# Kernel optimization log

Hardware: AMD Instinct MI355X
Metric: run time of the kernel (lower is better)

The kernel has to match this reference:

```python
import jax, jax.numpy as jnp
import numpy as np

B, F, V, E, D_DENSE = 16384, 26, 100000, 16, 13
HIDDEN = [256, 128]
DNN_IN = F * E + D_DENSE  # 429
INIT_STD = 1e-4


def setup_inputs() -> dict:
    key = jax.random.key(0)
    ks = jax.random.split(key, 12)
    X_sparse = jax.random.randint(ks[0], (B, F), 0, V, dtype=jnp.int32)
    X_dense = jax.random.normal(ks[1], (B, D_DENSE), dtype=jnp.float32)
    # Per-field embedding tables stacked: [F, V, dim]
    lin_emb_w = jax.random.normal(ks[2], (F, V, 1), dtype=jnp.float32) * 0.01
    fm_emb_w = jax.random.normal(ks[3], (F, V, E), dtype=jnp.float32) * 0.01
    dense_w = jax.random.normal(ks[4], (1, D_DENSE), dtype=jnp.float32) * 0.01
    dense_b = jnp.zeros((1,), dtype=jnp.float32)
    W1 = jax.random.normal(ks[5], (HIDDEN[0], DNN_IN), dtype=jnp.float32) * INIT_STD
    b1 = jnp.zeros((HIDDEN[0],), dtype=jnp.float32)
    W2 = jax.random.normal(ks[6], (HIDDEN[1], HIDDEN[0]), dtype=jnp.float32) * INIT_STD
    b2 = jnp.zeros((HIDDEN[1],), dtype=jnp.float32)
    Wout = jax.random.normal(ks[7], (1, HIDDEN[1]), dtype=jnp.float32) * 0.01
    return {"X_sparse": X_sparse, "X_dense": X_dense, "lin_emb_w": lin_emb_w,
            "fm_emb_w": fm_emb_w, "dense_w": dense_w, "dense_b": dense_b,
            "W1": W1, "b1": b1, "W2": W2, "b2": b2, "Wout": Wout}


def reference(X_sparse, X_dense, lin_emb_w, fm_emb_w, dense_w, dense_b,
              W1, b1, W2, b2, Wout):
    f_idx = jnp.arange(F)[None, :]  # broadcast field index against [B, F]
    # --- FM linear (1st order) part ---
    lin_sparse = lin_emb_w[f_idx, X_sparse]            # [B, F, 1]
    lin_sparse = jnp.sum(lin_sparse, axis=1)           # [B, 1]
    lin_dense = X_dense @ dense_w.T + dense_b          # [B, 1]
    linear_part = lin_sparse + lin_dense
    # --- FM 2nd-order cross term ---
    fm = fm_emb_w[f_idx, X_sparse]                     # [B, F, E]
    sum_emb = jnp.sum(fm, axis=1)                      # [B, E]
    square_of_sum = sum_emb * sum_emb
    sum_of_square = jnp.sum(fm * fm, axis=1)
    cross = 0.5 * jnp.sum(square_of_sum - sum_of_square, axis=1, keepdims=True)
    fm_logit = linear_part + cross                     # [B, 1]
    # --- DNN part (dropout identity: eval mode) ---
    h = jnp.concatenate([fm.reshape(B, F * E), X_dense], axis=1)  # [B, 429]
    h = jax.nn.relu(h @ W1.T + b1)
    h = jax.nn.relu(h @ W2.T + b2)
    dnn_logit = h @ Wout.T                             # [B, 1]
    out = jax.nn.sigmoid(fm_logit + dnn_logit)
    return out.squeeze(1)                              # [B]
```

## Files before the change

kernel.cpp:

```cpp
#include <hip/hip_runtime.h>
#include <hip/hip_bf16.h>
#include <math.h>

#define BTOT   16384
#define NF     26
#define VOCAB  100000
#define EDIM   16
#define DD     13
#define KPAD   448
#define KREAL  429
#define N1     256
#define N2     128
#define SPB    32
#define APAD   456
#define H2PAD  264

typedef __attribute__((ext_vector_type(8))) short bf16x8;
typedef __attribute__((ext_vector_type(4))) short bf16x4;
typedef __attribute__((ext_vector_type(4))) float f32x4;

static __device__ __forceinline__ bf16x8 ldb8(const __hip_bfloat16* p) {
  return *reinterpret_cast<const bf16x8*>(p);
}
static __device__ __forceinline__ short f2bf(float f) {
  __hip_bfloat16 h = __float2bfloat16(f);
  return *reinterpret_cast<short*>(&h);
}

__global__ __launch_bounds__(512) void convert_weights(
    const float* __restrict__ W1, const float* __restrict__ W2,
    __hip_bfloat16* __restrict__ W1f, __hip_bfloat16* __restrict__ W2f) {
  const int bid = blockIdx.x;
  const int k = threadIdx.x;
  if (bid < 256) {
    const int n = bid;
    if (k < 448) {
      float v = (k < KREAL) ? W1[(size_t)n * KREAL + k] : 0.f;
      W1f[(((size_t)(k >> 3)) * N1 + n) * 8 + (k & 7)] = __float2bfloat16(v);
    }
  } else {
    const int n = bid - 256;
    if (k < 256) {
      float v = W2[(size_t)n * 256 + k];
      W2f[(((size_t)(k >> 3)) * N2 + n) * 8 + (k & 7)] = __float2bfloat16(v);
    }
  }
}

__global__ __launch_bounds__(1024, 8) void deepfm_fused(
    const int* __restrict__ Xs, const float* __restrict__ Xd,
    const float* __restrict__ linW, const float* __restrict__ fmW,
    const float* __restrict__ denseW, const float* __restrict__ denseB,
    const __hip_bfloat16* __restrict__ W1f, const float* __restrict__ b1,
    const __hip_bfloat16* __restrict__ W2f, const float* __restrict__ b2,
    const float* __restrict__ Wout, float* __restrict__ out) {

  __shared__ __hip_bfloat16 Ash[SPB][APAD];
  __shared__ __hip_bfloat16 H2sh[SPB][H2PAD];
  __shared__ float fmlsh[SPB];
  __shared__ float redsh[SPB][8];

  const int tid = threadIdx.x;
  const size_t blk0 = (size_t)blockIdx.x * SPB;

  {
    const int s   = tid >> 5;
    const int sub = tid & 31;
    const int q   = sub & 3;
    const int g   = sub >> 2;
    const size_t b = blk0 + s;
    const int* xrow = Xs + b * NF;

    int idxs[4];
#pragma unroll
    for (int i = 0; i < 4; ++i) {
      int f = g + 8 * i;
      idxs[i] = (f < NF) ? xrow[f] : 0;
    }

    f32x4 sum = (f32x4){0.f, 0.f, 0.f, 0.f};
    f32x4 sumsq = (f32x4){0.f, 0.f, 0.f, 0.f};
    float part = 0.f;

#pragma unroll
    for (int i = 0; i < 4; ++i) {
      const int f = g + 8 * i;
      if (f < NF) {
        const float* row = fmW + ((size_t)f * VOCAB + idxs[i]) * EDIM;
        f32x4 v = *reinterpret_cast<const f32x4*>(row + q * 4);
        sum += v;
        sumsq += v * v;
        bf16x4 pk;
        pk[0] = f2bf(v[0]); pk[1] = f2bf(v[1]);
        pk[2] = f2bf(v[2]); pk[3] = f2bf(v[3]);
        *reinterpret_cast<bf16x4*>(&Ash[s][f * EDIM + q * 4]) = pk;
        if (q == (i & 3))
          part += linW[(size_t)f * VOCAB + idxs[i]];
      }
    }
#pragma unroll
    for (int off = 4; off <= 16; off <<= 1) {
#pragma unroll
      for (int c = 0; c < 4; ++c) {
        sum[c] += __shfl_xor(sum[c], off);
        sumsq[c] += __shfl_xor(sumsq[c], off);
      }
    }
    if (g == 0) {
      f32x4 c4 = sum * sum - sumsq;
      part += 0.5f * (c4[0] + c4[1] + c4[2] + c4[3]);
    }
    float xd = (sub < DD) ? Xd[b * DD + sub] : 0.f;
    Ash[s][416 + sub] = __float2bfloat16(xd);
    if (sub < DD) part += xd * denseW[sub];
#pragma unroll
    for (int off = 1; off < 32; off <<= 1)
      part += __shfl_xor(part, off);
    if (sub == 0) fmlsh[s] = part + denseB[0];
  }
  __syncthreads();

  const int wave = tid >> 6;
  const int lane = tid & 63;
  const int lr = lane & 15;
  const int kg = lane >> 4;
  {
    const int n0 = wave * 16;
    f32x4 acc[2];
    acc[0] = (f32x4){0.f, 0.f, 0.f, 0.f};
    acc[1] = (f32x4){0.f, 0.f, 0.f, 0.f};

#pragma unroll
    for (int kt = 0; kt < KPAD / 32; ++kt) {
      const int kbase = kt * 32 + kg * 8;
      bf16x8 bf = ldb8(W1f + ((size_t)(kbase >> 3) * N1 + n0 + lr) * 8);
#pragma unroll
      for (int mt = 0; mt < 2; ++mt) {
        bf16x8 af = *reinterpret_cast<const bf16x8*>(&Ash[mt * 16 + lr][kbase]);
        acc[mt] = __builtin_amdgcn_mfma_f32_16x16x32_bf16(af, bf, acc[mt], 0, 0, 0);
      }
    }
    const int col = n0 + lr;
    const float bias = b1[col];
#pragma unroll
    for (int mt = 0; mt < 2; ++mt) {
#pragma unroll
      for (int r = 0; r < 4; ++r) {
        float v = acc[mt][r] + bias;
        v = v > 0.f ? v : 0.f;
        H2sh[mt * 16 + kg * 4 + r][col] = __float2bfloat16(v);
      }
    }
  }
  __syncthreads();

  {
    const int c  = wave & 7;
    const int h  = wave >> 3;
    const int n0 = c * 16;
    f32x4 acc = (f32x4){0.f, 0.f, 0.f, 0.f};

#pragma unroll
    for (int kt = 0; kt < N1 / 32; ++kt) {
      const int kbase = kt * 32 + kg * 8;
      bf16x8 bf = ldb8(W2f + ((size_t)(kbase >> 3) * N2 + n0 + lr) * 8);
      bf16x8 af = *reinterpret_cast<const bf16x8*>(&H2sh[h * 16 + lr][kbase]);
      acc = __builtin_amdgcn_mfma_f32_16x16x32_bf16(af, bf, acc, 0, 0, 0);
    }
    const float w0 = Wout[n0 + lr];
    const float bb0 = b2[n0 + lr];
#pragma unroll
    for (int r = 0; r < 4; ++r) {
      float v = acc[r] + bb0;
      v = v > 0.f ? v : 0.f;
      v *= w0;
#pragma unroll
      for (int off = 1; off < 16; off <<= 1)
        v += __shfl_xor(v, off);
      if (lr == 0) redsh[h * 16 + kg * 4 + r][c] = v;
    }
  }
  __syncthreads();

  if (tid < SPB) {
    const int row = tid;
    float t = 0.f;
#pragma unroll
    for (int w = 0; w < 8; ++w) t += redsh[row][w];
    float x = fmlsh[row] + t;
    out[blk0 + row] = 1.f / (1.f + expf(-x));
  }
}

extern "C" void kernel_launch(void* const* d_in, const int* in_sizes, int n_in,
                              void* d_out, int out_size, void* d_ws, size_t ws_size,
                              hipStream_t stream) {
  const int*   Xs   = (const int*)d_in[0];
  const float* Xd   = (const float*)d_in[1];
  const float* linW = (const float*)d_in[2];
  const float* fmW  = (const float*)d_in[3];
  const float* dW   = (const float*)d_in[4];
  const float* dB   = (const float*)d_in[5];
  const float* W1   = (const float*)d_in[6];
  const float* b1   = (const float*)d_in[7];
  const float* W2   = (const float*)d_in[8];
  const float* b2   = (const float*)d_in[9];
  const float* Wout = (const float*)d_in[10];
  float* out = (float*)d_out;

  char* ws = (char*)d_ws;
  __hip_bfloat16* W1f = (__hip_bfloat16*)(ws);
  __hip_bfloat16* W2f = (__hip_bfloat16*)(ws + 229376);

  convert_weights<<<384, 512, 0, stream>>>(W1, W2, W1f, W2f);
  deepfm_fused<<<BTOT / SPB, 1024, 0, stream>>>(
      Xs, Xd, linW, fmW, dW, dB, W1f, b1, W2f, b2, Wout, out);
}
```

Measured before the change: 34.36 us.

## Halve block size and overlap embedding gather with MLP stages across waves

The block shrinks from 1024 to 512 threads and its 32 samples are processed in two halves of 16. While waves 0-3 gather embeddings for the second half, waves 4-7 run the first GEMM on the first half. Next, waves 0-3 run GEMM1 on the second half while waves 4-7 run GEMM2 on the first. All waves then finish GEMM2 for the second half. The aim is to hide the latency of the random embedding gathers behind MFMA work. The cost is more work per wave (four N tiles each), more block phases, and the first gather phase still running alone.

```diff
diff --git a/kernel.cpp b/kernel.cpp
--- a/kernel.cpp
+++ b/kernel.cpp
@@ -47,7 +47,83 @@
   }
 }
 
-__global__ __launch_bounds__(1024, 8) void deepfm_fused(
+
+__device__ __forceinline__ void gemm1_chunk(
+    int r0, int w4, int lane,
+    const __hip_bfloat16 (*Ash)[APAD], __hip_bfloat16 (*H2sh)[H2PAD],
+    const __hip_bfloat16* __restrict__ W1f, const float* __restrict__ b1) {
+  const int lr = lane & 15;
+  const int kg = lane >> 4;
+  const int n0 = w4 * 64;
+  f32x4 acc[4];
+#pragma unroll
+  for (int nt = 0; nt < 4; ++nt) acc[nt] = (f32x4){0.f, 0.f, 0.f, 0.f};
+
+#pragma unroll
+  for (int kt = 0; kt < KPAD / 32; ++kt) {
+    const int kbase = kt * 32 + kg * 8;
+    bf16x8 af = *reinterpret_cast<const bf16x8*>(&Ash[r0 + lr][kbase]);
+#pragma unroll
+    for (int nt = 0; nt < 4; ++nt) {
+      bf16x8 bf = ldb8(W1f + ((size_t)(kbase >> 3) * N1 + n0 + nt * 16 + lr) * 8);
+      acc[nt] = __builtin_amdgcn_mfma_f32_16x16x32_bf16(af, bf, acc[nt], 0, 0, 0);
+    }
+  }
+#pragma unroll
+  for (int nt = 0; nt < 4; ++nt) {
+    const int col = n0 + nt * 16 + lr;
+    const float bias = b1[col];
+#pragma unroll
+    for (int r = 0; r < 4; ++r) {
+      float v = acc[nt][r] + bias;
+      v = v > 0.f ? v : 0.f;
+      H2sh[r0 + kg * 4 + r][col] = __float2bfloat16(v);
+    }
+  }
+}
+
+template <int NWAVES>
+__device__ __forceinline__ void gemm2_chunk(
+    int r0, int wl, int lane,
+    const __hip_bfloat16 (*H2sh)[H2PAD], float (*redsh)[8],
+    const __hip_bfloat16* __restrict__ W2f, const float* __restrict__ b2,
+    const float* __restrict__ Wout) {
+  const int lr = lane & 15;
+  const int kg = lane >> 4;
+  constexpr int NT = 128 / (16 * NWAVES);
+  const int n0 = wl * NT * 16;
+  f32x4 acc[NT];
+#pragma unroll
+  for (int nt = 0; nt < NT; ++nt) acc[nt] = (f32x4){0.f, 0.f, 0.f, 0.f};
+
+#pragma unroll
+  for (int kt = 0; kt < N1 / 32; ++kt) {
+    const int kbase = kt * 32 + kg * 8;
+    bf16x8 af = *reinterpret_cast<const bf16x8*>(&H2sh[r0 + lr][kbase]);
+#pragma unroll
+    for (int nt = 0; nt < NT; ++nt) {
+      bf16x8 bf = ldb8(W2f + ((size_t)(kbase >> 3) * N2 + n0 + nt * 16 + lr) * 8);
+      acc[nt] = __builtin_amdgcn_mfma_f32_16x16x32_bf16(af, bf, acc[nt], 0, 0, 0);
+    }
+  }
+#pragma unroll
+  for (int r = 0; r < 4; ++r) {
+    float v = 0.f;
+#pragma unroll
+    for (int nt = 0; nt < NT; ++nt) {
+      const int col = n0 + nt * 16 + lr;
+      float t = acc[nt][r] + b2[col];
+      t = t > 0.f ? t : 0.f;
+      v += t * Wout[col];
+    }
+#pragma unroll
+    for (int off = 1; off < 16; off <<= 1)
+      v += __shfl_xor(v, off);
+    if (lr == 0) redsh[r0 + kg * 4 + r][wl] = v;
+  }
+}
+
+__global__ __launch_bounds__(512, 4) void deepfm_fused(
     const int* __restrict__ Xs, const float* __restrict__ Xd,
     const float* __restrict__ linW, const float* __restrict__ fmW,
     const float* __restrict__ denseW, const float* __restrict__ denseB,
@@ -61,6 +137,8 @@
   __shared__ float redsh[SPB][8];
 
   const int tid = threadIdx.x;
+  const int wave = tid >> 6;
+  const int lane = tid & 63;
   const size_t blk0 = (size_t)blockIdx.x * SPB;
 
   {
@@ -77,19 +155,71 @@
       int f = g + 8 * i;
       idxs[i] = (f < NF) ? xrow[f] : 0;
     }
-
     f32x4 sum = (f32x4){0.f, 0.f, 0.f, 0.f};
     f32x4 sumsq = (f32x4){0.f, 0.f, 0.f, 0.f};
     float part = 0.f;
-
 #pragma unroll
     for (int i = 0; i < 4; ++i) {
       const int f = g + 8 * i;
       if (f < NF) {
         const float* row = fmW + ((size_t)f * VOCAB + idxs[i]) * EDIM;
         f32x4 v = *reinterpret_cast<const f32x4*>(row + q * 4);
-        sum += v;
-        sumsq += v * v;
+        sum += v; sumsq += v * v;
+        bf16x4 pk;
+        pk[0] = f2bf(v[0]); pk[1] = f2bf(v[1]);
+        pk[2] = f2bf(v[2]); pk[3] = f2bf(v[3]);
+        *reinterpret_cast<bf16x4*>(&Ash[s][f * EDIM + q * 4]) = pk;
+        if (q == i)
+          part += linW[(size_t)f * VOCAB + idxs[i]];
+      }
+    }
+#pragma unroll
+    for (int off = 4; off <= 16; off <<= 1) {
+#pragma unroll
+      for (int c = 0; c < 4; ++c) {
+        sum[c] += __shfl_xor(sum[c], off);
+        sumsq[c] += __shfl_xor(sumsq[c], off);
+      }
+    }
+    if (g == 0) {
+      f32x4 c4 = sum * sum - sumsq;
+      part += 0.5f * (c4[0] + c4[1] + c4[2] + c4[3]);
+    }
+    float xd = (sub < DD) ? Xd[b * DD + sub] : 0.f;
+    Ash[s][416 + sub] = __float2bfloat16(xd);
+    if (sub < DD) part += xd * denseW[sub];
+#pragma unroll
+    for (int off = 1; off < 32; off <<= 1)
+      part += __shfl_xor(part, off);
+    if (sub == 0) fmlsh[s] = part + denseB[0];
+  }
+  __syncthreads();
+
+  if (wave < 4) {
+    const int t   = tid;
+    const int s   = 16 + (t >> 4);
+    const int sub = t & 15;
+    const int q   = sub & 3;
+    const int g   = sub >> 2;
+    const size_t b = blk0 + s;
+    const int* xrow = Xs + b * NF;
+
+    int idxs[7];
+#pragma unroll
+    for (int i = 0; i < 7; ++i) {
+      int f = g + 4 * i;
+      idxs[i] = (f < NF) ? xrow[f] : 0;
+    }
+    f32x4 sum = (f32x4){0.f, 0.f, 0.f, 0.f};
+    f32x4 sumsq = (f32x4){0.f, 0.f, 0.f, 0.f};
+    float part = 0.f;
+#pragma unroll
+    for (int i = 0; i < 7; ++i) {
+      const int f = g + 4 * i;
+      if (f < NF) {
+        const float* row = fmW + ((size_t)f * VOCAB + idxs[i]) * EDIM;
+        f32x4 v = *reinterpret_cast<const f32x4*>(row + q * 4);
+        sum += v; sumsq += v * v;
         bf16x4 pk;
         pk[0] = f2bf(v[0]); pk[1] = f2bf(v[1]);
         pk[2] = f2bf(v[2]); pk[3] = f2bf(v[3]);
@@ -99,7 +229,7 @@
       }
     }
 #pragma unroll
-    for (int off = 4; off <= 16; off <<= 1) {
+    for (int off = 4; off <= 8; off <<= 1) {
 #pragma unroll
       for (int c = 0; c < 4; ++c) {
         sum[c] += __shfl_xor(sum[c], off);
@@ -112,81 +242,32 @@
     }
     float xd = (sub < DD) ? Xd[b * DD + sub] : 0.f;
     Ash[s][416 + sub] = __float2bfloat16(xd);
+    Ash[s][432 + sub] = __float2bfloat16(0.f);
     if (sub < DD) part += xd * denseW[sub];
 #pragma unroll
-    for (int off = 1; off < 32; off <<= 1)
+    for (int off = 1; off < 16; off <<= 1)
       part += __shfl_xor(part, off);
     if (sub == 0) fmlsh[s] = part + denseB[0];
-  }
-  __syncthreads();
-
-  const int wave = tid >> 6;
-  const int lane = tid & 63;
-  const int lr = lane & 15;
-  const int kg = lane >> 4;
-  {
-    const int n0 = wave * 16;
-    f32x4 acc[2];
-    acc[0] = (f32x4){0.f, 0.f, 0.f, 0.f};
-    acc[1] = (f32x4){0.f, 0.f, 0.f, 0.f};
-
-#pragma unroll
-    for (int kt = 0; kt < KPAD / 32; ++kt) {
-      const int kbase = kt * 32 + kg * 8;
-      bf16x8 bf = ldb8(W1f + ((size_t)(kbase >> 3) * N1 + n0 + lr) * 8);
-#pragma unroll
-      for (int mt = 0; mt < 2; ++mt) {
-        bf16x8 af = *reinterpret_cast<const bf16x8*>(&Ash[mt * 16 + lr][kbase]);
-        acc[mt] = __builtin_amdgcn_mfma_f32_16x16x32_bf16(af, bf, acc[mt], 0, 0, 0);
-      }
-    }
-    const int col = n0 + lr;
-    const float bias = b1[col];
-#pragma unroll
-    for (int mt = 0; mt < 2; ++mt) {
-#pragma unroll
-      for (int r = 0; r < 4; ++r) {
-        float v = acc[mt][r] + bias;
-        v = v > 0.f ? v : 0.f;
-        H2sh[mt * 16 + kg * 4 + r][col] = __float2bfloat16(v);
-      }
-    }
-  }
-  __syncthreads();
-
-  {
-    const int c  = wave & 7;
-    const int h  = wave >> 3;
-    const int n0 = c * 16;
-    f32x4 acc = (f32x4){0.f, 0.f, 0.f, 0.f};
-
-#pragma unroll
-    for (int kt = 0; kt < N1 / 32; ++kt) {
-      const int kbase = kt * 32 + kg * 8;
-      bf16x8 bf = ldb8(W2f + ((size_t)(kbase >> 3) * N2 + n0 + lr) * 8);
-      bf16x8 af = *reinterpret_cast<const bf16x8*>(&H2sh[h * 16 + lr][kbase]);
-      acc = __builtin_amdgcn_mfma_f32_16x16x32_bf16(af, bf, acc, 0, 0, 0);
-    }
-    const float w0 = Wout[n0 + lr];
-    const float bb0 = b2[n0 + lr];
-#pragma unroll
-    for (int r = 0; r < 4; ++r) {
-      float v = acc[r] + bb0;
-      v = v > 0.f ? v : 0.f;
-      v *= w0;
-#pragma unroll
-      for (int off = 1; off < 16; off <<= 1)
-        v += __shfl_xor(v, off);
-      if (lr == 0) redsh[h * 16 + kg * 4 + r][c] = v;
-    }
-  }
+  } else {
+    gemm1_chunk(0, wave - 4, lane, Ash, H2sh, W1f, b1);
+  }
+  __syncthreads();
+
+  if (wave < 4) {
+    gemm1_chunk(16, wave, lane, Ash, H2sh, W1f, b1);
+  } else {
+    gemm2_chunk<4>(0, wave - 4, lane, H2sh, redsh, W2f, b2, Wout);
+  }
+  __syncthreads();
+
+  gemm2_chunk<8>(16, wave, lane, H2sh, redsh, W2f, b2, Wout);
   __syncthreads();
 
   if (tid < SPB) {
     const int row = tid;
+    const int nslots = (row < 16) ? 4 : 8;
     float t = 0.f;
-#pragma unroll
-    for (int w = 0; w < 8; ++w) t += redsh[row][w];
+    for (int w = 0; w < nslots; ++w) t += redsh[row][w];
     float x = fmlsh[row] + t;
     out[blk0 + row] = 1.f / (1.f + expf(-x));
   }
@@ -213,6 +294,6 @@
   __hip_bfloat16* W2f = (__hip_bfloat16*)(ws + 229376);
 
   convert_weights<<<384, 512, 0, stream>>>(W1, W2, W1f, W2f);
-  deepfm_fused<<<BTOT / SPB, 1024, 0, stream>>>(
+  deepfm_fused<<<BTOT / SPB, 512, 0, stream>>>(
       Xs, Xd, linW, fmW, dW, dB, W1f, b1, W2f, b2, Wout, out);
 }
```

Measured after the change: 35.85 us. 4.4% more time.

## Process two sample tiles per block and prefetch the second tile's gathers

Applied to the files above, without the earlier changes.

Each block now handles 64 samples as two 32-sample tiles. The embedding gathers for both tiles are issued up front, so the second tile's gather latency can hide behind the first tile's MLP GEMMs. The first tile's barriers wait only on LDS traffic (lgkmcnt), not on the outstanding global loads. This halves the grid and lowers the launch-bounds occupancy hint, and it raises register pressure, which may reduce latency hiding across blocks.

```diff
diff --git a/kernel.cpp b/kernel.cpp
--- a/kernel.cpp
+++ b/kernel.cpp
@@ -11,7 +11,6 @@
 #define KREAL  429
 #define N1     256
 #define N2     128
-#define SPB    32
 #define APAD   456
 #define H2PAD  264
 
@@ -26,6 +25,12 @@
   __hip_bfloat16 h = __float2bfloat16(f);
   return *reinterpret_cast<short*>(&h);
 }
+
+#define LGKM_BAR() do {                                   \
+  asm volatile("s_waitcnt lgkmcnt(0)" ::: "memory");      \
+  __builtin_amdgcn_s_barrier();                           \
+  asm volatile("" ::: "memory");                          \
+} while (0)
 
 __global__ __launch_bounds__(512) void convert_weights(
     const float* __restrict__ W1, const float* __restrict__ W2,
@@ -47,148 +52,199 @@
   }
 }
 
-__global__ __launch_bounds__(1024, 8) void deepfm_fused(
+__device__ __forceinline__ void gather_issue(
+    int g, int q, const int idxs[4],
+    const float* __restrict__ fmW, const float* __restrict__ linW,
+    f32x4 v[4], float& lin) {
+  lin = 0.f;
+#pragma unroll
+  for (int i = 0; i < 4; ++i) {
+    const int f = g + 8 * i;
+    if (f < NF) {
+      v[i] = *reinterpret_cast<const f32x4*>(
+          fmW + ((size_t)f * VOCAB + idxs[i]) * EDIM + q * 4);
+      if (q == i)
+        lin = linW[(size_t)f * VOCAB + idxs[i]];
+    }
+  }
+}
+
+__device__ __forceinline__ void build_tile(
+    int s, int sub, int q, int g, const f32x4 v[4], float lin, float xd,
+    const float* __restrict__ denseW, const float* __restrict__ denseB,
+    __hip_bfloat16 (*Ash)[APAD], float* __restrict__ fml_slot) {
+  f32x4 sum = (f32x4){0.f, 0.f, 0.f, 0.f};
+  f32x4 sumsq = (f32x4){0.f, 0.f, 0.f, 0.f};
+  float part = lin;
+#pragma unroll
+  for (int i = 0; i < 4; ++i) {
+    const int f = g + 8 * i;
+    if (f < NF) {
+      f32x4 vv = v[i];
+      sum += vv;
+      sumsq += vv * vv;
+      bf16x4 pk;
+      pk[0] = f2bf(vv[0]); pk[1] = f2bf(vv[1]);
+      pk[2] = f2bf(vv[2]); pk[3] = f2bf(vv[3]);
+      *reinterpret_cast<bf16x4*>(&Ash[s][f * EDIM + q * 4]) = pk;
+    }
+  }
+#pragma unroll
+  for (int off = 4; off <= 16; off <<= 1) {
+#pragma unroll
+    for (int c = 0; c < 4; ++c) {
+      sum[c] += __shfl_xor(sum[c], off);
+      sumsq[c] += __shfl_xor(sumsq[c], off);
+    }
+  }
+  if (g == 0) {
+    f32x4 c4 = sum * sum - sumsq;
+    part += 0.5f * (c4[0] + c4[1] + c4[2] + c4[3]);
+  }
+  Ash[s][416 + sub] = __float2bfloat16(xd);
+  if (sub < DD) part += xd * denseW[sub];
+#pragma unroll
+  for (int off = 1; off < 32; off <<= 1)
+    part += __shfl_xor(part, off);
+  if (sub == 0) fml_slot[s] = part + denseB[0];
+}
+
+__device__ __forceinline__ void gemm1_32(
+    int wave, int lr, int kg,
+    const __hip_bfloat16 (*Ash)[APAD], __hip_bfloat16 (*H2sh)[H2PAD],
+    const __hip_bfloat16* __restrict__ W1f, const float* __restrict__ bias1) {
+  const int n0 = wave * 16;
+  f32x4 acc[2];
+  acc[0] = (f32x4){0.f, 0.f, 0.f, 0.f};
+  acc[1] = (f32x4){0.f, 0.f, 0.f, 0.f};
+#pragma unroll
+  for (int kt = 0; kt < KPAD / 32; ++kt) {
+    const int kbase = kt * 32 + kg * 8;
+    bf16x8 bf = ldb8(W1f + ((size_t)(kbase >> 3) * N1 + n0 + lr) * 8);
+#pragma unroll
+    for (int mt = 0; mt < 2; ++mt) {
+      bf16x8 af = *reinterpret_cast<const bf16x8*>(&Ash[mt * 16 + lr][kbase]);
+      acc[mt] = __builtin_amdgcn_mfma_f32_16x16x32_bf16(af, bf, acc[mt], 0, 0, 0);
+    }
+  }
+  const int col = n0 + lr;
+  const float bias = bias1[col];
+#pragma unroll
+  for (int mt = 0; mt < 2; ++mt) {
+#pragma unroll
+    for (int r = 0; r < 4; ++r) {
+      float v = acc[mt][r] + bias;
+      v = v > 0.f ? v : 0.f;
+      H2sh[mt * 16 + kg * 4 + r][col] = __float2bfloat16(v);
+    }
+  }
+}
+
+__device__ __forceinline__ void gemm2_32(
+    int wave, int lr, int kg,
+    const __hip_bfloat16 (*H2sh)[H2PAD], float (*redsh)[8],
+    const __hip_bfloat16* __restrict__ W2f, const float* __restrict__ bias2,
+    const float* __restrict__ Wout) {
+  const int c = wave & 7;
+  const int h = wave >> 3;
+  const int n0 = c * 16;
+  f32x4 acc = (f32x4){0.f, 0.f, 0.f, 0.f};
+#pragma unroll
+  for (int kt = 0; kt < N1 / 32; ++kt) {
+    const int kbase = kt * 32 + kg * 8;
+    bf16x8 bf = ldb8(W2f + ((size_t)(kbase >> 3) * N2 + n0 + lr) * 8);
+    bf16x8 af = *reinterpret_cast<const bf16x8*>(&H2sh[h * 16 + lr][kbase]);
+    acc = __builtin_amdgcn_mfma_f32_16x16x32_bf16(af, bf, acc, 0, 0, 0);
+  }
+  const float w0 = Wout[n0 + lr];
+  const float bb0 = bias2[n0 + lr];
+#pragma unroll
+  for (int r = 0; r < 4; ++r) {
+    float v = acc[r] + bb0;
+    v = v > 0.f ? v : 0.f;
+    v *= w0;
+#pragma unroll
+    for (int off = 1; off < 16; off <<= 1)
+      v += __shfl_xor(v, off);
+    if (lr == 0) redsh[h * 16 + kg * 4 + r][c] = v;
+  }
+}
+
+__global__ __launch_bounds__(1024, 4) void deepfm_fused(
     const int* __restrict__ Xs, const float* __restrict__ Xd,
     const float* __restrict__ linW, const float* __restrict__ fmW,
     const float* __restrict__ denseW, const float* __restrict__ denseB,
-    const __hip_bfloat16* __restrict__ W1f, const float* __restrict__ b1,
-    const __hip_bfloat16* __restrict__ W2f, const float* __restrict__ b2,
+    const __hip_bfloat16* __restrict__ W1f, const float* __restrict__ bias1,
+    const __hip_bfloat16* __restrict__ W2f, const float* __restrict__ bias2,
     const float* __restrict__ Wout, float* __restrict__ out) {
 
-  __shared__ __hip_bfloat16 Ash[SPB][APAD];
-  __shared__ __hip_bfloat16 H2sh[SPB][H2PAD];
-  __shared__ float fmlsh[SPB];
-  __shared__ float redsh[SPB][8];
+  __shared__ __hip_bfloat16 Ash[32][APAD];
+  __shared__ __hip_bfloat16 H2sh[32][H2PAD];
+  __shared__ float fmlsh[64];
+  __shared__ float redsh[32][8];
 
   const int tid = threadIdx.x;
-  const size_t blk0 = (size_t)blockIdx.x * SPB;
-
-  {
-    const int s   = tid >> 5;
-    const int sub = tid & 31;
-    const int q   = sub & 3;
-    const int g   = sub >> 2;
-    const size_t b = blk0 + s;
-    const int* xrow = Xs + b * NF;
-
-    int idxs[4];
-#pragma unroll
-    for (int i = 0; i < 4; ++i) {
-      int f = g + 8 * i;
-      idxs[i] = (f < NF) ? xrow[f] : 0;
-    }
-
-    f32x4 sum = (f32x4){0.f, 0.f, 0.f, 0.f};
-    f32x4 sumsq = (f32x4){0.f, 0.f, 0.f, 0.f};
-    float part = 0.f;
-
-#pragma unroll
-    for (int i = 0; i < 4; ++i) {
-      const int f = g + 8 * i;
-      if (f < NF) {
-        const float* row = fmW + ((size_t)f * VOCAB + idxs[i]) * EDIM;
-        f32x4 v = *reinterpret_cast<const f32x4*>(row + q * 4);
-        sum += v;
-        sumsq += v * v;
-        bf16x4 pk;
-        pk[0] = f2bf(v[0]); pk[1] = f2bf(v[1]);
-        pk[2] = f2bf(v[2]); pk[3] = f2bf(v[3]);
-        *reinterpret_cast<bf16x4*>(&Ash[s][f * EDIM + q * 4]) = pk;
-        if (q == (i & 3))
-          part += linW[(size_t)f * VOCAB + idxs[i]];
-      }
-    }
-#pragma unroll
-    for (int off = 4; off <= 16; off <<= 1) {
-#pragma unroll
-      for (int c = 0; c < 4; ++c) {
-        sum[c] += __shfl_xor(sum[c], off);
-        sumsq[c] += __shfl_xor(sumsq[c], off);
-      }
-    }
-    if (g == 0) {
-      f32x4 c4 = sum * sum - sumsq;
-      part += 0.5f * (c4[0] + c4[1] + c4[2] + c4[3]);
-    }
-    float xd = (sub < DD) ? Xd[b * DD + sub] : 0.f;
-    Ash[s][416 + sub] = __float2bfloat16(xd);
-    if (sub < DD) part += xd * denseW[sub];
-#pragma unroll
-    for (int off = 1; off < 32; off <<= 1)
-      part += __shfl_xor(part, off);
-    if (sub == 0) fmlsh[s] = part + denseB[0];
-  }
-  __syncthreads();
-
   const int wave = tid >> 6;
   const int lane = tid & 63;
   const int lr = lane & 15;
   const int kg = lane >> 4;
-  {
-    const int n0 = wave * 16;
-    f32x4 acc[2];
-    acc[0] = (f32x4){0.f, 0.f, 0.f, 0.f};
-    acc[1] = (f32x4){0.f, 0.f, 0.f, 0.f};
-
-#pragma unroll
-    for (int kt = 0; kt < KPAD / 32; ++kt) {
-      const int kbase = kt * 32 + kg * 8;
-      bf16x8 bf = ldb8(W1f + ((size_t)(kbase >> 3) * N1 + n0 + lr) * 8);
-#pragma unroll
-      for (int mt = 0; mt < 2; ++mt) {
-        bf16x8 af = *reinterpret_cast<const bf16x8*>(&Ash[mt * 16 + lr][kbase]);
-        acc[mt] = __builtin_amdgcn_mfma_f32_16x16x32_bf16(af, bf, acc[mt], 0, 0, 0);
-      }
-    }
-    const int col = n0 + lr;
-    const float bias = b1[col];
-#pragma unroll
-    for (int mt = 0; mt < 2; ++mt) {
-#pragma unroll
-      for (int r = 0; r < 4; ++r) {
-        float v = acc[mt][r] + bias;
-        v = v > 0.f ? v : 0.f;
-        H2sh[mt * 16 + kg * 4 + r][col] = __float2bfloat16(v);
-      }
-    }
-  }
+  const size_t blk0 = (size_t)blockIdx.x * 64;
+
+  const int s   = tid >> 5;
+  const int sub = tid & 31;
+  const int q   = sub & 3;
+  const int g   = sub >> 2;
+  const size_t sb0 = blk0 + s;
+  const size_t sb1 = sb0 + 32;
+
+  const int* xr0 = Xs + sb0 * NF;
+  const int* xr1 = Xs + sb1 * NF;
+  int idx0[4], idx1[4];
+#pragma unroll
+  for (int i = 0; i < 4; ++i) {
+    const int f = g + 8 * i;
+    idx0[i] = (f < NF) ? xr0[f] : 0;
+    idx1[i] = (f < NF) ? xr1[f] : 0;
+  }
+  float xd0 = (sub < DD) ? Xd[sb0 * DD + sub] : 0.f;
+  float xd1 = (sub < DD) ? Xd[sb1 * DD + sub] : 0.f;
+
+  f32x4 v0[4]; float lin0;
+  gather_issue(g, q, idx0, fmW, linW, v0, lin0);
+  f32x4 v1[4]; float lin1;
+  gather_issue(g, q, idx1, fmW, linW, v1, lin1);
+
+  build_tile(s, sub, q, g, v0, lin0, xd0, denseW, denseB, Ash, fmlsh);
+  LGKM_BAR();
+
+  gemm1_32(wave, lr, kg, Ash, H2sh, W1f, bias1);
+  LGKM_BAR();
+
+  gemm2_32(wave, lr, kg, H2sh, redsh, W2f, bias2, Wout);
+  LGKM_BAR();
+
+  if (tid < 32) {
+    float t = 0.f;
+#pragma unroll
+    for (int w = 0; w < 8; ++w) t += redsh[tid][w];
+    float x = fmlsh[tid] + t;
+    out[blk0 + tid] = 1.f / (1.f + expf(-x));
+  }
+  build_tile(s, sub, q, g, v1, lin1, xd1, denseW, denseB, Ash, fmlsh + 32);
   __syncthreads();
 
-  {
-    const int c  = wave & 7;
-    const int h  = wave >> 3;
-    const int n0 = c * 16;
-    f32x4 acc = (f32x4){0.f, 0.f, 0.f, 0.f};
-
-#pragma unroll
-    for (int kt = 0; kt < N1 / 32; ++kt) {
-      const int kbase = kt * 32 + kg * 8;
-      bf16x8 bf = ldb8(W2f + ((size_t)(kbase >> 3) * N2 + n0 + lr) * 8);
-      bf16x8 af = *reinterpret_cast<const bf16x8*>(&H2sh[h * 16 + lr][kbase]);
-      acc = __builtin_amdgcn_mfma_f32_16x16x32_bf16(af, bf, acc, 0, 0, 0);
-    }
-    const float w0 = Wout[n0 + lr];
-    const float bb0 = b2[n0 + lr];
-#pragma unroll
-    for (int r = 0; r < 4; ++r) {
-      float v = acc[r] + bb0;
-      v = v > 0.f ? v : 0.f;
-      v *= w0;
-#pragma unroll
-      for (int off = 1; off < 16; off <<= 1)
-        v += __shfl_xor(v, off);
-      if (lr == 0) redsh[h * 16 + kg * 4 + r][c] = v;
-    }
-  }
+  gemm1_32(wave, lr, kg, Ash, H2sh, W1f, bias1);
   __syncthreads();
 
-  if (tid < SPB) {
-    const int row = tid;
+  gemm2_32(wave, lr, kg, H2sh, redsh, W2f, bias2, Wout);
+  __syncthreads();
+
+  if (tid < 32) {
     float t = 0.f;
 #pragma unroll
-    for (int w = 0; w < 8; ++w) t += redsh[row][w];
-    float x = fmlsh[row] + t;
-    out[blk0 + row] = 1.f / (1.f + expf(-x));
+    for (int w = 0; w < 8; ++w) t += redsh[tid][w];
+    float x = fmlsh[32 + tid] + t;
+    out[blk0 + 32 + tid] = 1.f / (1.f + expf(-x));
   }
 }
 
@@ -213,6 +269,6 @@
   __hip_bfloat16* W2f = (__hip_bfloat16*)(ws + 229376);
 
   convert_weights<<<384, 512, 0, stream>>>(W1, W2, W1f, W2f);
-  deepfm_fused<<<BTOT / SPB, 1024, 0, stream>>>(
+  deepfm_fused<<<BTOT / 64, 1024, 0, stream>>>(
       Xs, Xd, linW, fmW, dW, dB, W1f, b1, W2f, b2, Wout, out);
 }
```

Result: slower. 36.18 us (+5.3%).
